# Optimization experiments

Hardware: AMD Instinct MI355X
Metric: run time of the kernel (lower is better)

Reference implementation:

```python
import jax, jax.numpy as jnp
import numpy as np

DIM = 384
WS = 7
N = WS * WS
H = 12
HD = DIM // H
SCALE = HD ** -0.5
B_ = 4096
NW = 64


def _rel_pos_index():
    ii, jj = np.meshgrid(np.arange(WS), np.arange(WS), indexing='ij')
    flat = np.stack([ii.ravel(), jj.ravel()])  # [2, N]
    rel = flat[:, :, None] - flat[:, None, :]  # [2, N, N]
    rel = rel.transpose(1, 2, 0)
    rel[:, :, 0] += WS - 1
    rel[:, :, 1] += WS - 1
    rel[:, :, 0] *= 2 * WS - 1
    return jnp.asarray(rel.sum(-1), dtype=jnp.int32)  # [N, N]


def setup_inputs() -> dict:
    key = jax.random.key(0)
    ks = jax.random.split(key, 7)
    return {
        'x': jax.random.normal(ks[0], (B_, N, DIM), dtype=jnp.float32),
        'mask': jax.random.normal(ks[1], (NW, N, N), dtype=jnp.float32),
        'qkv_w': jax.random.normal(ks[2], (3 * DIM, DIM), dtype=jnp.float32) * 0.02,
        'qkv_b': jax.random.normal(ks[3], (3 * DIM,), dtype=jnp.float32) * 0.02,
        'proj_w': jax.random.normal(ks[4], (DIM, DIM), dtype=jnp.float32) * 0.02,
        'proj_b': jax.random.normal(ks[5], (DIM,), dtype=jnp.float32) * 0.02,
        'rel_bias_table': jax.random.normal(ks[6], ((2 * WS - 1) ** 2, H), dtype=jnp.float32) * 0.02,
        'rel_pos_index': _rel_pos_index(),
    }


def reference(x, mask, qkv_w, qkv_b, proj_w, proj_b, rel_bias_table, rel_pos_index):
    b_, n, c = x.shape
    h, hd = H, c // H
    qkv = x @ qkv_w.T + qkv_b  # [B_, N, 3C]
    qkv = qkv.reshape(b_, n, 3, h, hd)
    q, k, v = qkv[:, :, 0], qkv[:, :, 1], qkv[:, :, 2]  # [B_, N, H, hd]
    attn = jnp.einsum('bnhd,bmhd->bhnm', q, k) * SCALE  # [B_, H, N, N]
    bias = rel_bias_table[rel_pos_index]  # [N, N, H]
    attn = attn + jnp.transpose(bias, (2, 0, 1))[None]
    nw = mask.shape[0]
    attn = attn.reshape(b_ // nw, nw, h, n, n) + mask[None, :, None]
    attn = attn.reshape(b_, h, n, n)
    attn = jax.nn.softmax(attn, axis=-1)
    out = jnp.einsum('bhnm,bmhd->bnhd', attn, v).reshape(b_, n, c)
    return out @ proj_w.T + proj_b
```

## Files before the change

### kernel.cpp

```cpp
#include <hip/hip_runtime.h>
#include <hip/hip_bf16.h>

typedef __attribute__((ext_vector_type(4))) float  f32x4;
typedef __attribute__((ext_vector_type(8))) short  s16x8;

#define DEVI static __device__ __forceinline__

constexpr int   BQ    = 4096;
constexpr int   NTOK  = 49;
constexpr int   DIMC  = 384;
constexpr int   NH    = 12;
constexpr int   HDIM  = 32;
constexpr int   NW    = 64;
constexpr int   QKVN  = 3 * DIMC;
constexpr float SCALE_ = 0.17677669529663687f;
constexpr float LOG2E  = 1.4426950408889634f;

DEVI ushort f2bf(float f) {
  union { float f; unsigned u; } v; v.f = f;
  unsigned r = v.u + 0x7fffu + ((v.u >> 16) & 1u);
  return (ushort)(r >> 16);
}

DEVI float fexp2(float x) {
  float r;
  asm("v_exp_f32 %0, %1" : "=v"(r) : "v"(x));
  return r;
}

DEVI void async_ld16(const ushort* g, const ushort* l) {
  auto gp = reinterpret_cast<const __attribute__((address_space(1))) unsigned int*>(
      reinterpret_cast<uintptr_t>(g));
  auto lp = reinterpret_cast<__attribute__((address_space(3))) unsigned int*>(
      reinterpret_cast<uintptr_t>(l));
  __builtin_amdgcn_global_load_lds(gp, lp, 16, 0, 0);
}

constexpr int PREP_N1 = QKVN * DIMC;
constexpr int PREP_N2 = DIMC * DIMC;
constexpr int PREP_N3 = NW * NH * 16 * 64;
constexpr int PREP_N4 = QKVN;
constexpr int PREP_TOT    = PREP_N1 + PREP_N2 + PREP_N3 + PREP_N4;
constexpr int PREP_BLOCKS = (PREP_TOT + 255) / 256;
constexpr int CAST_BLOCKS = 2048;
__global__ void prep_cast_kernel(const float* __restrict__ qkv_w, const float* __restrict__ proj_w,
                                 const float* __restrict__ tab, const int* __restrict__ idx,
                                 const float* __restrict__ mask, const float* __restrict__ qkv_b,
                                 ushort* __restrict__ qw, ushort* __restrict__ pw,
                                 float* __restrict__ combP, float* __restrict__ qbias,
                                 const float* __restrict__ x, ushort* __restrict__ xb, int n8) {
  if (blockIdx.x >= PREP_BLOCKS) {
    int i = (blockIdx.x - PREP_BLOCKS) * 256 + threadIdx.x;
    const int stride = CAST_BLOCKS * 256;
    for (; i < n8; i += stride) {
      f32x4 a = *(const f32x4*)(x + (size_t)i * 8);
      f32x4 b = *(const f32x4*)(x + (size_t)i * 8 + 4);
      s16x8 v;
      v[0] = (short)f2bf(a[0]); v[1] = (short)f2bf(a[1]);
      v[2] = (short)f2bf(a[2]); v[3] = (short)f2bf(a[3]);
      v[4] = (short)f2bf(b[0]); v[5] = (short)f2bf(b[1]);
      v[6] = (short)f2bf(b[2]); v[7] = (short)f2bf(b[3]);
      *(s16x8*)(xb + (size_t)i * 8) = v;
    }
    return;
  }
  int i = blockIdx.x * 256 + threadIdx.x;
  if (i < PREP_N1) {
    int n = i / DIMC;
    float sc = (n < DIMC) ? SCALE_ : 1.0f;
    qw[i] = f2bf(qkv_w[i] * sc);
  } else if (i < PREP_N1 + PREP_N2) {
    int j = i - PREP_N1;
    pw[j] = f2bf(proj_w[j]);
  } else if (i < PREP_N1 + PREP_N2 + PREP_N3) {
    int j = i - PREP_N1 - PREP_N2;
    int lane = j & 63;
    int tile = (j >> 6) & 15;
    int wh   = j >> 10;
    int h = wh % NH, w = wh / NH;
    int it = tile >> 2, jt = tile & 3;
    int c = jt * 16 + (lane & 15);
    f32x4 v;
    #pragma unroll
    for (int r = 0; r < 4; r++) {
      int rr = it * 16 + (lane >> 4) * 4 + r;
      v[r] = (rr < NTOK && c < NTOK)
           ? (tab[idx[rr * NTOK + c] * NH + h] + mask[(size_t)w * NTOK * NTOK + rr * NTOK + c]) * LOG2E
           : -1.0e30f;
    }
    ((f32x4*)combP)[j] = v;
  } else if (i < PREP_TOT) {
    int j = i - PREP_N1 - PREP_N2 - PREP_N3;
    qbias[j] = qkv_b[j] * ((j < DIMC) ? SCALE_ : 1.0f);
  }
}

template<int EPI, int K, int NB>
__global__ __launch_bounds__(256) void gemm_bt_kernel(
    const ushort* __restrict__ Ap, const ushort* __restrict__ Bp,
    const float* __restrict__ bias, float* __restrict__ outF,
    ushort* __restrict__ Qb, ushort* __restrict__ Kb, ushort* __restrict__ Vb)
{
  struct MB { ushort A[3][256 * 32]; ushort B[3][128 * 32]; };
  union ShU { MB mb; ushort Ct[2][128 * 136]; };
  __shared__ ShU sh;

  const int tid  = threadIdx.x;
  const int lane = tid & 63;
  const int wv   = tid >> 6;
  const int wm   = (wv >> 1) * 128, wn = (wv & 1) * 64;
  const int l15  = lane & 15, lg = lane >> 4;
  const int swz  = (l15 >> 1) & 3;
  constexpr int NT = NB * 128;

  const int chunk = gridDim.x >> 3;
  const int wgid  = (blockIdx.x & 7) * chunk + (blockIdx.x >> 3);
  const int nbase = (wgid % NB) * 128;
  const int mbase = (wgid / NB) * 256;

  const int srow = lane >> 2;
  const int scol = (((lane & 3) ^ ((srow >> 1) & 3)) * 8);

  const ushort* Abase = Ap + (size_t)(mbase + wv * 64 + srow) * K + scol;
  const ushort* Bbase = Bp + (size_t)(nbase + wv * 32 + srow) * K + scol;

  f32x4 acc[8][4];
  #pragma unroll
  for (int i = 0; i < 8; i++)
    #pragma unroll
    for (int j = 0; j < 4; j++) acc[i][j] = (f32x4){0.f, 0.f, 0.f, 0.f};

  auto stage = [&](int buf, int k0) {
    #pragma unroll
    for (int i = 0; i < 4; i++)
      async_ld16(Abase + (size_t)i * 16 * K + k0, &sh.mb.A[buf][(wv * 64 + i * 16) * 32]);
    #pragma unroll
    for (int i = 0; i < 2; i++)
      async_ld16(Bbase + (size_t)i * 16 * K + k0, &sh.mb.B[buf][(wv * 32 + i * 16) * 32]);
  };
  auto compute = [&](int buf) {
    s16x8 bfv[4];
    #pragma unroll
    for (int t = 0; t < 4; t++)
      bfv[t] = *(const s16x8*)&sh.mb.B[buf][(wn + t*16 + l15) * 32 + ((lg ^ swz) << 3)];
    #pragma unroll
    for (int mt = 0; mt < 8; mt++) {
      s16x8 af = *(const s16x8*)&sh.mb.A[buf][(wm + mt*16 + l15) * 32 + ((lg ^ swz) << 3)];
      #pragma unroll
      for (int nt = 0; nt < 4; nt++)
        acc[mt][nt] = __builtin_amdgcn_mfma_f32_16x16x32_bf16(af, bfv[nt], acc[mt][nt], 0, 0, 0);
    }
  };

  constexpr int NSTEP = K / 32;
  stage(0, 0);
  stage(1, 32);
  #pragma unroll
  for (int t = 0; t < NSTEP; t++) {
    if (t + 1 < NSTEP) { asm volatile("s_waitcnt vmcnt(6)" ::: "memory"); }
    else               { asm volatile("s_waitcnt vmcnt(0)" ::: "memory"); }
    __builtin_amdgcn_s_barrier();
    asm volatile("" ::: "memory");
    __builtin_amdgcn_sched_barrier(0);
    if (t + 2 < NSTEP) stage((t + 2) % 3, (t + 2) * 32);
    compute(t % 3);
  }

  if (EPI == 0) {
    #pragma unroll
    for (int mt = 0; mt < 8; mt++)
      #pragma unroll
      for (int nt = 0; nt < 4; nt++) {
        int n = nbase + wn + nt*16 + l15;
        float bv = bias[n];
        #pragma unroll
        for (int r = 0; r < 4; r++) {
          int m = mbase + wm + mt*16 + lg*4 + r;
          outF[(size_t)m * NT + n] = acc[mt][nt][r] + bv;
        }
      }
  } else {
    __syncthreads();
    float bv[4];
    #pragma unroll
    for (int nt = 0; nt < 4; nt++) bv[nt] = bias[nbase + wn + nt*16 + l15];
    const int half = wv >> 1;
    #pragma unroll
    for (int mt = 0; mt < 8; mt++)
      #pragma unroll
      for (int nt = 0; nt < 4; nt++) {
        int col = wn + nt*16 + l15;
        #pragma unroll
        for (int r = 0; r < 4; r++)
          sh.Ct[half][(mt*16 + lg*4 + r) * 136 + col] = f2bf(acc[mt][nt][r] + bv[nt]);
      }
    __syncthreads();
    const int which = nbase / DIMC;
    const int h0    = (nbase - which * DIMC) >> 5;
    ushort* obase = (which == 0) ? Qb : (which == 1) ? Kb : Vb;
    #pragma unroll
    for (int i = 0; i < 16; i++) {
      int c    = tid + i * 256;
      int hs   = c >> 10;
      int j    = c & 1023;
      int rloc = j >> 2;
      int d0   = (j & 3) * 8;
      int m = mbase + rloc;
      int b = m / NTOK, tok = m - b * NTOK;
      *(s16x8*)(obase + (((size_t)b * NH + h0 + hs) * NTOK + tok) * HDIM + d0) =
          *(const s16x8*)&sh.Ct[rloc >> 7][(rloc & 127) * 136 + hs * 32 + d0];
    }
  }
}

__global__ __launch_bounds__(64) void attn_kernel(
    const ushort* __restrict__ Qb, const ushort* __restrict__ Kb,
    const ushort* __restrict__ Vb, const float* __restrict__ combP,
    ushort* __restrict__ Ob)
{
  __shared__ ushort PV[64][72];
  const int bid  = blockIdx.x;
  const int b    = bid >> 2;
  const int wv   = bid & 3;
  const int lane = threadIdx.x;
  const int l15  = lane & 15, lg = lane >> 4;
  const int widx = b & (NW - 1);

  for (int hi = 0; hi < 3; hi++) {
    const int h = wv * 3 + hi;
    const ushort* Qh = Qb + ((size_t)b * NH + h) * NTOK * HDIM;
    const ushort* Kh = Kb + ((size_t)b * NH + h) * NTOK * HDIM;
    const ushort* Vh = Vb + ((size_t)b * NH + h) * NTOK * HDIM;
    const f32x4*  cp = (const f32x4*)combP + ((size_t)widx * NH + h) * (16 * 64) + lane;

    s16x8 qf[4], kf[4];
    #pragma unroll
    for (int t = 0; t < 4; t++) {
      int r = t*16 + l15; r = r > 48 ? 48 : r;
      qf[t] = *(const s16x8*)(Qh + r*HDIM + lg*8);
      kf[t] = *(const s16x8*)(Kh + r*HDIM + lg*8);
    }

    {
      s16x8 vrow[4];
      #pragma unroll
      for (int c = 0; c < 4; c++)
        vrow[c] = (lane < NTOK) ? *(const s16x8*)(Vh + (size_t)lane*HDIM + c*8)
                                : (s16x8){0,0,0,0,0,0,0,0};
      #pragma unroll
      for (int c = 0; c < 4; c++)
        #pragma unroll
        for (int e = 0; e < 8; e++)
          PV[c*8 + e][lane] = (ushort)vrow[c][e];
    }

    s16x8 vf[2][2];
    #pragma unroll
    for (int nt = 0; nt < 2; nt++)
      #pragma unroll
      for (int kk = 0; kk < 2; kk++)
        vf[nt][kk] = *(const s16x8*)&PV[nt*16 + l15][kk*32 + lg*8];
    asm volatile("s_waitcnt lgkmcnt(0)" ::: "memory");
    __builtin_amdgcn_sched_barrier(0);

    f32x4 rsum[4];
    #pragma unroll
    for (int it = 0; it < 4; it++) {
      const int RM = (it == 3) ? 1 : 4;
      f32x4 sr[4];
      __builtin_amdgcn_s_setprio(1);
      #pragma unroll
      for (int jt = 0; jt < 4; jt++)
        sr[jt] = __builtin_amdgcn_mfma_f32_16x16x32_bf16(qf[it], kf[jt],
                                                         (f32x4){0.f,0.f,0.f,0.f}, 0, 0, 0);
      __builtin_amdgcn_s_setprio(0);

      f32x4 rs = (f32x4){0.f, 0.f, 0.f, 0.f};
      #pragma unroll
      for (int jt = 0; jt < 4; jt++) {
        f32x4 cadd = cp[(it*4 + jt) * 64];
        #pragma unroll
        for (int r = 0; r < RM; r++) {
          float e = fexp2(__builtin_fmaf(sr[jt][r], LOG2E, cadd[r]));
          rs[r] += e;
          PV[it*16 + lg*4 + r][jt*16 + l15] = f2bf(e);
        }
      }
      #pragma unroll
      for (int r = 0; r < RM; r++)
        #pragma unroll
        for (int x = 1; x < 16; x <<= 1)
          rs[r] += __shfl_xor(rs[r], x);
      rsum[it] = rs;
    }

    f32x4 o[4][2];
    #pragma unroll
    for (int it = 0; it < 4; it++)
      #pragma unroll
      for (int nt = 0; nt < 2; nt++) o[it][nt] = (f32x4){0.f,0.f,0.f,0.f};
    __builtin_amdgcn_s_setprio(1);
    #pragma unroll
    for (int it = 0; it < 4; it++)
      #pragma unroll
      for (int kk = 0; kk < 2; kk++) {
        s16x8 pf = *(const s16x8*)&PV[it*16 + l15][kk*32 + lg*8];
        #pragma unroll
        for (int nt = 0; nt < 2; nt++)
          o[it][nt] = __builtin_amdgcn_mfma_f32_16x16x32_bf16(pf, vf[nt][kk], o[it][nt], 0, 0, 0);
      }
    __builtin_amdgcn_s_setprio(0);

    #pragma unroll
    for (int it = 0; it < 4; it++)
      #pragma unroll
      for (int r = 0; r < 4; r++) {
        int q = it*16 + lg*4 + r;
        if (q < NTOK) {
          float ri = 1.0f / rsum[it][r];
          #pragma unroll
          for (int nt = 0; nt < 2; nt++)
            Ob[((size_t)b*NTOK + q)*DIMC + h*HDIM + nt*16 + l15] = f2bf(o[it][nt][r] * ri);
        }
      }
  }
}

extern "C" void kernel_launch(void* const* d_in, const int* in_sizes, int n_in,
                              void* d_out, int out_size, void* d_ws, size_t ws_size,
                              hipStream_t stream)
{
  const float* x      = (const float*)d_in[0];
  const float* mask   = (const float*)d_in[1];
  const float* qkv_w  = (const float*)d_in[2];
  const float* qkv_b  = (const float*)d_in[3];
  const float* proj_w = (const float*)d_in[4];
  const float* proj_b = (const float*)d_in[5];
  const float* rtab   = (const float*)d_in[6];
  const int*   ridx   = (const int*)d_in[7];
  float* out = (float*)d_out;

  char* p = (char*)d_ws;
  auto alloc = [&](size_t bytes) { char* r = p; p += (bytes + 255) & ~(size_t)255; return r; };
  ushort* xb    = (ushort*)alloc((size_t)BQ*NTOK*DIMC*2);
  ushort* Qb    = (ushort*)alloc((size_t)BQ*NH*NTOK*HDIM*2);
  ushort* Kb    = (ushort*)alloc((size_t)BQ*NH*NTOK*HDIM*2);
  ushort* Vb    = (ushort*)alloc((size_t)BQ*NH*NTOK*HDIM*2);
  ushort* Ob    = (ushort*)alloc((size_t)BQ*NTOK*DIMC*2);
  ushort* qw    = (ushort*)alloc((size_t)QKVN*DIMC*2);
  ushort* pw    = (ushort*)alloc((size_t)DIMC*DIMC*2);
  float*  cbP   = (float*)alloc((size_t)NW*NH*16*64*4*4);
  float*  qbias = (float*)alloc((size_t)QKVN*4);

  const int n8 = BQ*NTOK*DIMC/8;
  prep_cast_kernel<<<PREP_BLOCKS + CAST_BLOCKS, 256, 0, stream>>>(
      qkv_w, proj_w, rtab, ridx, mask, qkv_b, qw, pw, cbP, qbias, x, xb, n8);

  gemm_bt_kernel<1, DIMC, 9><<<7056, 256, 0, stream>>>(xb, qw, qbias, nullptr, Qb, Kb, Vb);

  attn_kernel<<<BQ * 4, 64, 0, stream>>>(Qb, Kb, Vb, cbP, Ob);

  gemm_bt_kernel<0, DIMC, 3><<<2352, 256, 0, stream>>>(Ob, pw, proj_b, out, nullptr, nullptr, nullptr);
}
```

Measured before the change: 665.0 us.

## Pre-swizzle GEMM weights to MFMA fragment layout and load B directly to registers

The weight-prep step now writes qkv and proj weights in a fragment-major layout, so each lane can load its MFMA B operand straight from global memory into registers, double-buffered two k-steps ahead. This removes B from shared memory. The epilogue staging is split into two halves that reuse a single Ct buffer. Together these shrink LDS use so launch_bounds can ask for 3 blocks per CU, aiming at higher occupancy and fewer LDS reads and writes. The cost is more register pressure, per-lane global loads of B, and an extra barrier in the epilogue.

```diff
diff --git a/kernel.cpp b/kernel.cpp
--- a/kernel.cpp
+++ b/kernel.cpp
@@ -66,12 +66,25 @@
   }
   int i = blockIdx.x * 256 + threadIdx.x;
   if (i < PREP_N1) {
-    int n = i / DIMC;
+    int e  = i & 7;
+    int l  = (i >> 3) & 63;
+    int g  = i >> 9;
+    int ks = g % 12;
+    int tl = g / 12;
+    int n  = tl * 16 + (l & 15);
+    int k  = ks * 32 + (l >> 4) * 8 + e;
     float sc = (n < DIMC) ? SCALE_ : 1.0f;
-    qw[i] = f2bf(qkv_w[i] * sc);
+    qw[i] = f2bf(qkv_w[n * DIMC + k] * sc);
   } else if (i < PREP_N1 + PREP_N2) {
-    int j = i - PREP_N1;
-    pw[j] = f2bf(proj_w[j]);
+    int j  = i - PREP_N1;
+    int e  = j & 7;
+    int l  = (j >> 3) & 63;
+    int g  = j >> 9;
+    int ks = g % 12;
+    int tl = g / 12;
+    int n  = tl * 16 + (l & 15);
+    int k  = ks * 32 + (l >> 4) * 8 + e;
+    pw[j] = f2bf(proj_w[n * DIMC + k]);
   } else if (i < PREP_N1 + PREP_N2 + PREP_N3) {
     int j = i - PREP_N1 - PREP_N2;
     int lane = j & 63;
@@ -96,15 +109,16 @@
 }
 
 template<int EPI, int K, int NB>
-__global__ __launch_bounds__(256) void gemm_bt_kernel(
+__global__ __launch_bounds__(256, 3) void gemm_bt_kernel(
     const ushort* __restrict__ Ap, const ushort* __restrict__ Bp,
     const float* __restrict__ bias, float* __restrict__ outF,
     ushort* __restrict__ Qb, ushort* __restrict__ Kb, ushort* __restrict__ Vb)
 {
-  struct MB { ushort A[3][256 * 32]; ushort B[3][128 * 32]; };
-  union ShU { MB mb; ushort Ct[2][128 * 136]; };
+  struct MB { ushort A[3][256 * 32]; };
+  union ShU { MB mb; ushort Ct[128 * 136]; };
   __shared__ ShU sh;
 
+  constexpr int NSTEP = K / 32;
   const int tid  = threadIdx.x;
   const int lane = tid & 63;
   const int wv   = tid >> 6;
@@ -122,7 +136,7 @@
   const int scol = (((lane & 3) ^ ((srow >> 1) & 3)) * 8);
 
   const ushort* Abase = Ap + (size_t)(mbase + wv * 64 + srow) * K + scol;
-  const ushort* Bbase = Bp + (size_t)(nbase + wv * 32 + srow) * K + scol;
+  const ushort* Bf = Bp + (((size_t)((nbase + wn) >> 4) * NSTEP) << 9) + lane * 8;
 
   f32x4 acc[8][4];
   #pragma unroll
@@ -134,15 +148,13 @@
     #pragma unroll
     for (int i = 0; i < 4; i++)
       async_ld16(Abase + (size_t)i * 16 * K + k0, &sh.mb.A[buf][(wv * 64 + i * 16) * 32]);
-    #pragma unroll
-    for (int i = 0; i < 2; i++)
-      async_ld16(Bbase + (size_t)i * 16 * K + k0, &sh.mb.B[buf][(wv * 32 + i * 16) * 32]);
   };
-  auto compute = [&](int buf) {
-    s16x8 bfv[4];
+  auto loadB = [&](int ks, s16x8* dst) {
     #pragma unroll
     for (int t = 0; t < 4; t++)
-      bfv[t] = *(const s16x8*)&sh.mb.B[buf][(wn + t*16 + l15) * 32 + ((lg ^ swz) << 3)];
+      dst[t] = *(const s16x8*)(Bf + ((size_t)(t * NSTEP + ks) << 9));
+  };
+  auto compute = [&](int buf, const s16x8* bfv) {
     #pragma unroll
     for (int mt = 0; mt < 8; mt++) {
       s16x8 af = *(const s16x8*)&sh.mb.A[buf][(wm + mt*16 + l15) * 32 + ((lg ^ swz) << 3)];
@@ -152,18 +164,21 @@
     }
   };
 
-  constexpr int NSTEP = K / 32;
+  s16x8 bfv0[4], bfv1[4];
+  loadB(0, bfv0);
   stage(0, 0);
+  loadB(1, bfv1);
   stage(1, 32);
   #pragma unroll
   for (int t = 0; t < NSTEP; t++) {
-    if (t + 1 < NSTEP) { asm volatile("s_waitcnt vmcnt(6)" ::: "memory"); }
+    if (t + 1 < NSTEP) { asm volatile("s_waitcnt vmcnt(8)" ::: "memory"); }
     else               { asm volatile("s_waitcnt vmcnt(0)" ::: "memory"); }
     __builtin_amdgcn_s_barrier();
     asm volatile("" ::: "memory");
     __builtin_amdgcn_sched_barrier(0);
     if (t + 2 < NSTEP) stage((t + 2) % 3, (t + 2) * 32);
-    compute(t % 3);
+    if (t & 1) { compute(t % 3, bfv1); if (t + 2 < NSTEP) loadB(t + 2, bfv1); }
+    else       { compute(t % 3, bfv0); if (t + 2 < NSTEP) loadB(t + 2, bfv0); }
   }
 
   if (EPI == 0) {
@@ -184,31 +199,37 @@
     float bv[4];
     #pragma unroll
     for (int nt = 0; nt < 4; nt++) bv[nt] = bias[nbase + wn + nt*16 + l15];
-    const int half = wv >> 1;
-    #pragma unroll
-    for (int mt = 0; mt < 8; mt++)
-      #pragma unroll
-      for (int nt = 0; nt < 4; nt++) {
-        int col = wn + nt*16 + l15;
-        #pragma unroll
-        for (int r = 0; r < 4; r++)
-          sh.Ct[half][(mt*16 + lg*4 + r) * 136 + col] = f2bf(acc[mt][nt][r] + bv[nt]);
-      }
-    __syncthreads();
     const int which = nbase / DIMC;
     const int h0    = (nbase - which * DIMC) >> 5;
     ushort* obase = (which == 0) ? Qb : (which == 1) ? Kb : Vb;
-    #pragma unroll
-    for (int i = 0; i < 16; i++) {
-      int c    = tid + i * 256;
-      int hs   = c >> 10;
-      int j    = c & 1023;
-      int rloc = j >> 2;
-      int d0   = (j & 3) * 8;
-      int m = mbase + rloc;
-      int b = m / NTOK, tok = m - b * NTOK;
-      *(s16x8*)(obase + (((size_t)b * NH + h0 + hs) * NTOK + tok) * HDIM + d0) =
-          *(const s16x8*)&sh.Ct[rloc >> 7][(rloc & 127) * 136 + hs * 32 + d0];
+    const int halfid = wv >> 1;
+    #pragma unroll
+    for (int half = 0; half < 2; half++) {
+      if (half) __syncthreads();
+      if (halfid == half) {
+        #pragma unroll
+        for (int mt = 0; mt < 8; mt++)
+          #pragma unroll
+          for (int nt = 0; nt < 4; nt++) {
+            int col = wn + nt*16 + l15;
+            #pragma unroll
+            for (int r = 0; r < 4; r++)
+              sh.Ct[(mt*16 + lg*4 + r) * 136 + col] = f2bf(acc[mt][nt][r] + bv[nt]);
+          }
+      }
+      __syncthreads();
+      #pragma unroll
+      for (int i = 0; i < 8; i++) {
+        int c    = tid + i * 256;
+        int hs   = c >> 9;
+        int j    = c & 511;
+        int rloc = j >> 2;
+        int d0   = (j & 3) * 8;
+        int m = mbase + half * 128 + rloc;
+        int b = m / NTOK, tok = m - b * NTOK;
+        *(s16x8*)(obase + (((size_t)b * NH + h0 + hs) * NTOK + tok) * HDIM + d0) =
+            *(const s16x8*)&sh.Ct[rloc * 136 + hs * 32 + d0];
+      }
     }
   }
 }
```

Result: slower. 1.642 ms (+146.9%).
